# Performance work log

Measured on AMD Instinct MI355X. Metric: run time of the kernel, lower is better.

Reference implementation:

```python
import jax, jax.numpy as jnp
import numpy as np

V_FEATS = 1024; N1 = 800; N2 = 800; K = 10
CONV = [256, 128]; DENSE = [256, 64]


def setup_inputs() -> dict:
    key = jax.random.key(0)
    ks = jax.random.split(key, 20)
    inp = {
        "Z1": jax.random.normal(ks[0], (N1, V_FEATS), jnp.float32),
        "nb1": jax.random.randint(ks[2], (N1, K), -1, N1),
        "Z2": jax.random.normal(ks[1], (N2, V_FEATS), jnp.float32),
        "nb2": jax.random.randint(ks[3], (N2, K), -1, N2),
    }
    j = 4
    dims = [V_FEATS] + CONV
    for i, (di, do) in enumerate(zip(dims[:-1], dims[1:])):
        s = 1.0 / np.sqrt(di)
        inp[f"Wr{i}"] = jax.random.normal(ks[j], (di, do), jnp.float32) * s; j += 1
        inp[f"Wnr{i}"] = jax.random.normal(ks[j], (di, do), jnp.float32) * s; j += 1
    fdims = [2 * CONV[-1]] + DENSE + [1]
    for i, (di, do) in enumerate(zip(fdims[:-1], fdims[1:])):
        s = 1.0 / np.sqrt(di)
        inp[f"fW{i}"] = jax.random.normal(ks[j], (di, do), jnp.float32) * s; j += 1
        inp[f"fb{i}"] = jnp.zeros((do,), jnp.float32)
    return inp


def gnn_layer(Z, nb, Wr, Wnr):
    # residue (self) signal and neighbor base signal
    res = Z @ Wr                                  # [N, F]
    base = Z @ Wnr                                # [N, F]
    mask = nb > -1                                # [N, K]
    feats = base[nb] * mask[..., None]            # gather (neg idx wrap, masked out)
    norm = jnp.maximum(mask.sum(1), 1).astype(Z.dtype)  # [N], avoid div-by-0
    return jax.nn.relu(res + feats.sum(1) / norm[:, None])


def _forward(Z1, nb1, Z2, nb2, Wr0, Wnr0, Wr1, Wnr1, fW0, fb0, fW1, fb1, fW2, fb2):
    # two stacked GNN layers per protein (shared weights across the two proteins)
    x1 = gnn_layer(gnn_layer(Z1, nb1, Wr0, Wnr0), nb1, Wr1, Wnr1)  # [N1, F]
    x2 = gnn_layer(gnn_layer(Z2, nb2, Wr0, Wnr0), nb2, Wr1, Wnr1)  # [N2, F]
    n1, F = x1.shape
    n2 = x2.shape[0]
    # all-pairs concat: itertools.product(rows(x1), rows(x2)) -> [N1*N2, 2F]
    pairs = jnp.concatenate(
        [jnp.broadcast_to(x1[:, None, :], (n1, n2, F)),
         jnp.broadcast_to(x2[None, :, :], (n1, n2, F))], axis=-1
    ).reshape(n1 * n2, 2 * F)
    h = jax.nn.relu(pairs @ fW0 + fb0)
    h = jax.nn.relu(h @ fW1 + fb1)
    return jnp.squeeze(h @ fW2 + fb2)             # [N1*N2]


def reference(Z1, nb1, Z2, nb2, Wr0, Wnr0, Wr1, Wnr1, fW0, fb0, fW1, fb1, fW2, fb2):
    return _forward(Z1, nb1, Z2, nb2, Wr0, Wnr0, Wr1, Wnr1,
                    fW0, fb0, fW1, fb1, fW2, fb2)
```

## Files before the change

### kernel.cpp

```cpp
#include <hip/hip_runtime.h>
#include <hip/hip_bf16.h>
#include <cstdint>
#include <cstddef>


typedef __bf16 bf16_t;
typedef __bf16 bf16x8 __attribute__((ext_vector_type(8)));
typedef float f32x4 __attribute__((ext_vector_type(4)));
typedef _Float16 f16_t;
typedef _Float16 f16x8 __attribute__((ext_vector_type(8)));

static __device__ __forceinline__ f32x4 mfma_bf16(bf16x8 a, bf16x8 b, f32x4 c) {
  return __builtin_amdgcn_mfma_f32_16x16x32_bf16(a, b, c, 0, 0, 0);
}
static __device__ __forceinline__ f32x4 mfma_f16(f16x8 a, f16x8 b, f32x4 c) {
  return __builtin_amdgcn_mfma_f32_16x16x32_f16(a, b, c, 0, 0, 0);
}

#define N1R 800
#define NR  1600
#define VF  1024
#define F0  256
#define F1  128

__global__ void conv_w(const float* __restrict__ Wr0, const float* __restrict__ Wnr0,
                       const float* __restrict__ Wr1, const float* __restrict__ Wnr1,
                       const float* __restrict__ fW0, const float* __restrict__ fW1,
                       const float* __restrict__ fb1, const float* __restrict__ fW2,
                       const float* __restrict__ fb2,
                       bf16_t* __restrict__ W0h, bf16_t* __restrict__ W0l,
                       bf16_t* __restrict__ W1h, bf16_t* __restrict__ W1l,
                       bf16_t* __restrict__ fAh, bf16_t* __restrict__ fAl,
                       bf16_t* __restrict__ fBh, bf16_t* __restrict__ fBl,
                       f16_t* __restrict__ fW1th, float* __restrict__ fbw) {
  int wb = blockIdx.x;
  if (wb >= 2560 && wb < 2624) {
    int t = (wb - 2560) * 256 + threadIdx.x;
    int n = t & 63;
    int k = t >> 6;
    fW1th[(n << 8) + k] = (f16_t)fW1[k * 64 + n];
    return;
  }
  if (wb == 2624) {
    int t = threadIdx.x;
    if (t < 128) {
      int jl = t & 15, s = t >> 4;
      fbw[jl * 8 + s] = (s < 4) ? fb1[s * 16 + jl] : fW2[(s - 4) * 16 + jl];
    } else if (t == 128) {
      fbw[128] = fb2[0];
    }
    return;
  }
  const float* src; bf16_t* dh; bf16_t* dl; int ld, lk, ln, b0;
  if      (wb < 1024) { src = Wr0;  ld = 256; lk = 10; ln = 8; dh = W0h;              dl = W0l;              b0 = 0;    }
  else if (wb < 2048) { src = Wnr0; ld = 256; lk = 10; ln = 8; dh = W0h + 256 * 1024; dl = W0l + 256 * 1024; b0 = 1024; }
  else if (wb < 2176) { src = Wr1;  ld = 128; lk = 8;  ln = 7; dh = W1h;              dl = W1l;              b0 = 2048; }
  else if (wb < 2304) { src = Wnr1; ld = 128; lk = 8;  ln = 7; dh = W1h + 128 * 256;  dl = W1l + 128 * 256;  b0 = 2176; }
  else if (wb < 2432) { src = fW0;             ld = 256; lk = 7; ln = 8; dh = fAh;    dl = fAl;              b0 = 2304; }
  else                { src = fW0 + 128 * 256; ld = 256; lk = 7; ln = 8; dh = fBh;    dl = fBl;              b0 = 2432; }
  int t = (wb - b0) * 256 + threadIdx.x;
  int n = t & ((1 << ln) - 1);
  int k = t >> ln;
  float v = src[k * ld + n];
  bf16_t h = (bf16_t)v;
  dh[(n << lk) + k] = h;
  dl[(n << lk) + k] = (bf16_t)(v - (float)h);
}

static __device__ __forceinline__ void split8(float4 va, float4 vb,
                                              bf16x8& h8, bf16x8& l8) {
  float v[8] = {va.x, va.y, va.z, va.w, vb.x, vb.y, vb.z, vb.w};
  #pragma unroll
  for (int e = 0; e < 8; ++e) {
    bf16_t h = (bf16_t)v[e];
    h8[e] = h;
    l8[e] = (bf16_t)(v[e] - (float)h);
  }
}

__global__ __launch_bounds__(256) void gemm_z(
    const float* __restrict__ Z1, const float* __restrict__ Z2,
    const bf16_t* __restrict__ Bth, const bf16_t* __restrict__ Btl,
    float* __restrict__ Cp, int kLen) {
  int lane = threadIdx.x & 63;
  int w = threadIdx.x >> 6;
  int wr = w >> 1, wc = w & 1;
  int jl = lane & 15, hi = lane >> 4;

  int row0 = blockIdx.y * 64 + wr * 32;
  int col0 = blockIdx.x * 64 + wc * 32;
  int z = blockIdx.z;
  int kStart = z * kLen;
  float* C = Cp + (size_t)z * NR * 512;

  int r0 = row0 + jl;
  int r1 = row0 + 16 + jl;
  int c0 = col0 + jl;
  int c1 = col0 + 16 + jl;

  const float* pZ0 = ((r0 < N1R) ? Z1 + (size_t)r0 * VF : Z2 + (size_t)(r0 - N1R) * VF) + hi * 8;
  const float* pZ1 = ((r1 < N1R) ? Z1 + (size_t)r1 * VF : Z2 + (size_t)(r1 - N1R) * VF) + hi * 8;
  const bf16_t* pB0h = Bth + (size_t)c0 * 1024 + hi * 8;
  const bf16_t* pB1h = Bth + (size_t)c1 * 1024 + hi * 8;
  const bf16_t* pB0l = Btl + (size_t)c0 * 1024 + hi * 8;
  const bf16_t* pB1l = Btl + (size_t)c1 * 1024 + hi * 8;

  f32x4 acc[2][2] = {};
  for (int kb = kStart; kb < kStart + kLen; kb += 32) {
    bf16x8 a0h, a0l, a1h, a1l;
    split8(*(const float4*)(pZ0 + kb), *(const float4*)(pZ0 + kb + 4), a0h, a0l);
    split8(*(const float4*)(pZ1 + kb), *(const float4*)(pZ1 + kb + 4), a1h, a1l);
    bf16x8 b0h = *(const bf16x8*)(pB0h + kb);
    bf16x8 b1h = *(const bf16x8*)(pB1h + kb);
    bf16x8 b0l = *(const bf16x8*)(pB0l + kb);
    bf16x8 b1l = *(const bf16x8*)(pB1l + kb);

    acc[0][0] = mfma_bf16(a0h, b0h, acc[0][0]);
    acc[0][1] = mfma_bf16(a0h, b1h, acc[0][1]);
    acc[1][0] = mfma_bf16(a1h, b0h, acc[1][0]);
    acc[1][1] = mfma_bf16(a1h, b1h, acc[1][1]);

    acc[0][0] = mfma_bf16(a0l, b0h, acc[0][0]);
    acc[0][1] = mfma_bf16(a0l, b1h, acc[0][1]);
    acc[1][0] = mfma_bf16(a1l, b0h, acc[1][0]);
    acc[1][1] = mfma_bf16(a1l, b1h, acc[1][1]);

    acc[0][0] = mfma_bf16(a0h, b0l, acc[0][0]);
    acc[0][1] = mfma_bf16(a0h, b1l, acc[0][1]);
    acc[1][0] = mfma_bf16(a1h, b0l, acc[1][0]);
    acc[1][1] = mfma_bf16(a1h, b1l, acc[1][1]);
  }

  #pragma unroll
  for (int m = 0; m < 2; ++m) {
    #pragma unroll
    for (int nn = 0; nn < 2; ++nn) {
      int col = col0 + nn * 16 + jl;
      #pragma unroll
      for (int reg = 0; reg < 4; ++reg) {
        int row = row0 + m * 16 + hi * 4 + reg;
        C[(size_t)row * 512 + col] = acc[m][nn][reg];
      }
    }
  }
}

static __device__ __forceinline__ void gemm_body(
    const bf16_t* __restrict__ Ah, const bf16_t* __restrict__ Al,
    const bf16_t* __restrict__ Bth, const bf16_t* __restrict__ Btl,
    const float* __restrict__ bias, float* __restrict__ C,
    f16_t* __restrict__ Ch,
    int M, int N, int K, int kStart, int kLen, int row0b, int col0b) {
  int lane = threadIdx.x & 63;
  int w = threadIdx.x >> 6;
  int wr = w >> 1, wc = w & 1;
  int jl = lane & 15, hi = lane >> 4;

  int row0 = row0b + wr * 32;
  int col0 = col0b + wc * 32;

  int r0 = min(row0 + jl, M - 1);
  int r1 = min(row0 + 16 + jl, M - 1);
  int c0 = col0 + jl;
  int c1 = col0 + 16 + jl;

  const bf16_t* pA0h = Ah + (size_t)r0 * K + hi * 8;
  const bf16_t* pA1h = Ah + (size_t)r1 * K + hi * 8;
  const bf16_t* pA0l = Al + (size_t)r0 * K + hi * 8;
  const bf16_t* pA1l = Al + (size_t)r1 * K + hi * 8;
  const bf16_t* pB0h = Bth + (size_t)c0 * K + hi * 8;
  const bf16_t* pB1h = Bth + (size_t)c1 * K + hi * 8;
  const bf16_t* pB0l = Btl + (size_t)c0 * K + hi * 8;
  const bf16_t* pB1l = Btl + (size_t)c1 * K + hi * 8;

  f32x4 acc[2][2] = {};
  for (int kb = kStart; kb < kStart + kLen; kb += 32) {
    bf16x8 a0h = *(const bf16x8*)(pA0h + kb);
    bf16x8 a1h = *(const bf16x8*)(pA1h + kb);
    bf16x8 a0l = *(const bf16x8*)(pA0l + kb);
    bf16x8 a1l = *(const bf16x8*)(pA1l + kb);
    bf16x8 b0h = *(const bf16x8*)(pB0h + kb);
    bf16x8 b1h = *(const bf16x8*)(pB1h + kb);
    bf16x8 b0l = *(const bf16x8*)(pB0l + kb);
    bf16x8 b1l = *(const bf16x8*)(pB1l + kb);

    acc[0][0] = mfma_bf16(a0h, b0h, acc[0][0]);
    acc[0][1] = mfma_bf16(a0h, b1h, acc[0][1]);
    acc[1][0] = mfma_bf16(a1h, b0h, acc[1][0]);
    acc[1][1] = mfma_bf16(a1h, b1h, acc[1][1]);

    acc[0][0] = mfma_bf16(a0l, b0h, acc[0][0]);
    acc[0][1] = mfma_bf16(a0l, b1h, acc[0][1]);
    acc[1][0] = mfma_bf16(a1l, b0h, acc[1][0]);
    acc[1][1] = mfma_bf16(a1l, b1h, acc[1][1]);

    acc[0][0] = mfma_bf16(a0h, b0l, acc[0][0]);
    acc[0][1] = mfma_bf16(a0h, b1l, acc[0][1]);
    acc[1][0] = mfma_bf16(a1h, b0l, acc[1][0]);
    acc[1][1] = mfma_bf16(a1h, b1l, acc[1][1]);
  }

  #pragma unroll
  for (int m = 0; m < 2; ++m) {
    #pragma unroll
    for (int nn = 0; nn < 2; ++nn) {
      int col = col0 + nn * 16 + jl;
      float bv = bias ? bias[col] : 0.f;
      #pragma unroll
      for (int reg = 0; reg < 4; ++reg) {
        int row = row0 + m * 16 + hi * 4 + reg;
        if (row < M) {
          float val = acc[m][nn][reg] + bv;
          if (Ch) Ch[(size_t)row * N + col] = (f16_t)val;
          else    C[(size_t)row * N + col] = val;
        }
      }
    }
  }
}

__global__ __launch_bounds__(256) void gemm_split(
    const bf16_t* __restrict__ Ah, const bf16_t* __restrict__ Al,
    const bf16_t* __restrict__ Bth, const bf16_t* __restrict__ Btl,
    float* __restrict__ Cp, int M, int N, int K, int kLen) {
  int z = blockIdx.z;
  gemm_body(Ah, Al, Bth, Btl, nullptr, Cp + (size_t)z * M * N, nullptr,
            M, N, K, z * kLen, kLen, blockIdx.y * 64, blockIdx.x * 64);
}

__global__ __launch_bounds__(256) void gemm_dual(
    const bf16_t* __restrict__ H1h, const bf16_t* __restrict__ H1l,
    const bf16_t* __restrict__ fAh, const bf16_t* __restrict__ fAl,
    const bf16_t* __restrict__ fBh, const bf16_t* __restrict__ fBl,
    const float* __restrict__ fb0, f16_t* __restrict__ ABh) {
  int part = blockIdx.y / 13;
  int my = blockIdx.y % 13;
  gemm_body(H1h + (size_t)part * N1R * F1, H1l + (size_t)part * N1R * F1,
            part ? fBh : fAh, part ? fBl : fAl, part ? nullptr : fb0,
            nullptr, ABh + (size_t)part * N1R * 256, N1R, 256, F1, 0, F1,
            my * 64, blockIdx.x * 64);
}

__global__ void agg_kernel(const float* __restrict__ RBp, const int* __restrict__ nb1,
                           const int* __restrict__ nb2, bf16_t* __restrict__ Hh,
                           bf16_t* __restrict__ Hl, int F, int S) {
  int row = blockIdx.x;
  int c = threadIdx.x;
  int Sw = 2 * F;
  const size_t P = (size_t)NR * Sw;
  const int* nb;
  int roff;
  if (row < N1R) { nb = nb1 + row * 10; roff = 0; }
  else           { nb = nb2 + (row - N1R) * 10; roff = N1R; }
  float s = 0.f; int cnt = 0;
  #pragma unroll
  for (int k = 0; k < 10; ++k) {
    int idx = nb[k];
    if (idx > -1) {
      cnt++;
      size_t o = (size_t)(roff + idx) * Sw + F + c;
      float t = 0.f;
      for (int z = 0; z < S; ++z) t += RBp[o + (size_t)z * P];
      s += t;
    }
  }
  size_t so = (size_t)row * Sw + c;
  float v = 0.f;
  for (int z = 0; z < S; ++z) v += RBp[so + (size_t)z * P];
  v += s / (float)(cnt > 0 ? cnt : 1);
  v = fmaxf(v, 0.f);
  bf16_t h = (bf16_t)v;
  Hh[(size_t)row * F + c] = h;
  Hl[(size_t)row * F + c] = (bf16_t)(v - (float)h);
}

#define IBLK 2
#define ITILE 16
__global__ __launch_bounds__(256) void pair_kernel(
    const f16_t* __restrict__ ABh, const f16_t* __restrict__ W1th,
    const float* __restrict__ fbw, float* __restrict__ out) {
  __shared__ alignas(16) unsigned char sWh[64 * 512];
  __shared__ alignas(16) f16_t sA[ITILE * 256];

  const int tid = threadIdx.x;
  const int lane = tid & 63;
  const int w = tid >> 6;
  const int jl = lane & 15;
  const int hi = lane >> 4;
  const int j0 = blockIdx.x * 64;
  const int i0 = blockIdx.y * ITILE;

  #pragma unroll
  for (int s = 0; s < 8; ++s) {
    int c = tid + 256 * s;
    int n = c >> 5;
    int cb = (c & 31) << 4;
    int sw = cb ^ ((n & 7) << 4);
    *(uint4*)(sWh + n * 512 + sw) = *(const uint4*)((const unsigned char*)W1th + n * 512 + cb);
  }
  #pragma unroll
  for (int s = 0; s < 2; ++s) {
    int c = tid + 256 * s;
    int rr = c >> 5;
    int cc = c & 31;
    *(uint4*)((unsigned char*)sA + rr * 512 + cc * 16) =
        *(const uint4*)(ABh + (size_t)(i0 + rr) * 256 + cc * 8);
  }

  int j = j0 + w * 16 + jl;
  f16x8 breg[8];
  {
    const f16_t* Bp = ABh + (size_t)(N1R + j) * 256;
    bool ok = (j < N1R);
    f16x8 z{};
    #pragma unroll
    for (int t = 0; t < 8; ++t)
      breg[t] = ok ? *(const f16x8*)(Bp + t * 32 + hi * 8) : z;
  }

  float4 fb1r = *(const float4*)(fbw + jl * 8);
  float4 fw2r = *(const float4*)(fbw + jl * 8 + 4);
  float bias2 = fbw[128];

  __syncthreads();

  #pragma unroll 1
  for (int ig = 0; ig < ITILE / IBLK; ++ig) {
    f32x4 acc[IBLK][4] = {};
    #pragma unroll
    for (int t = 0; t < 8; ++t) {
      f16x8 bv = breg[t];
      f16x8 af[IBLK];
      const f16x8 Zv{};
      #pragma unroll
      for (int ib = 0; ib < IBLK; ++ib) {
        f16x8 av = *(const f16x8*)(sA + (ig * IBLK + ib) * 256 + t * 32 + hi * 8);
        af[ib] = __builtin_elementwise_max(av + bv, Zv);
      }
      int kbyte = t * 64 + hi * 16;
      #pragma unroll
      for (int nf = 0; nf < 4; ++nf) {
        int n = nf * 16 + jl;
        f16x8 wh = *(const f16x8*)(sWh + n * 512 + (kbyte ^ ((n & 7) << 4)));
        #pragma unroll
        for (int ib = 0; ib < IBLK; ++ib)
          acc[ib][nf] = mfma_f16(af[ib], wh, acc[ib][nf]);
      }
    }
    float fb1a[4] = {fb1r.x, fb1r.y, fb1r.z, fb1r.w};
    float fw2a[4] = {fw2r.x, fw2r.y, fw2r.z, fw2r.w};
    #pragma unroll
    for (int ib = 0; ib < IBLK; ++ib) {
      float part[4];
      #pragma unroll
      for (int r = 0; r < 4; ++r) {
        float ssum = 0.f;
        #pragma unroll
        for (int nf = 0; nf < 4; ++nf) {
          float h = acc[ib][nf][r] + fb1a[nf];
          h = fmaxf(h, 0.f);
          ssum += h * fw2a[nf];
        }
        part[r] = ssum;
      }
      #pragma unroll
      for (int off = 1; off < 16; off <<= 1) {
        #pragma unroll
        for (int r = 0; r < 4; ++r) part[r] += __shfl_xor(part[r], off, 64);
      }
      if (jl == 0) {
        int jo = j0 + w * 16 + hi * 4;
        if (jo < N1R) {
          float4 o = make_float4(part[0] + bias2, part[1] + bias2,
                                 part[2] + bias2, part[3] + bias2);
          *(float4*)(out + (size_t)(i0 + ig * IBLK + ib) * 800 + jo) = o;
        }
      }
    }
  }
}

extern "C" void kernel_launch(void* const* d_in, const int* in_sizes, int n_in,
                              void* d_out, int out_size, void* d_ws, size_t ws_size,
                              hipStream_t stream) {
  const float* Z1   = (const float*)d_in[0];
  const int*   nb1  = (const int*)d_in[1];
  const float* Z2   = (const float*)d_in[2];
  const int*   nb2  = (const int*)d_in[3];
  const float* Wr0  = (const float*)d_in[4];
  const float* Wnr0 = (const float*)d_in[5];
  const float* Wr1  = (const float*)d_in[6];
  const float* Wnr1 = (const float*)d_in[7];
  const float* fW0  = (const float*)d_in[8];
  const float* fb0  = (const float*)d_in[9];
  const float* fW1  = (const float*)d_in[10];
  const float* fb1  = (const float*)d_in[11];
  const float* fW2  = (const float*)d_in[12];
  const float* fb2  = (const float*)d_in[13];
  float* out = (float*)d_out;

  char* p = (char*)d_ws;
  auto alloc = [&](size_t bytes) {
    char* q = p;
    p += (bytes + 255) & ~(size_t)255;
    return q;
  };
  bf16_t* W0h   = (bf16_t*)alloc((size_t)512 * 1024 * 2);
  bf16_t* W0l   = (bf16_t*)alloc((size_t)512 * 1024 * 2);
  bf16_t* W1h   = (bf16_t*)alloc((size_t)256 * 256 * 2);
  bf16_t* W1l   = (bf16_t*)alloc((size_t)256 * 256 * 2);
  bf16_t* fAh   = (bf16_t*)alloc((size_t)256 * 128 * 2);
  bf16_t* fAl   = (bf16_t*)alloc((size_t)256 * 128 * 2);
  bf16_t* fBh   = (bf16_t*)alloc((size_t)256 * 128 * 2);
  bf16_t* fBl   = (bf16_t*)alloc((size_t)256 * 128 * 2);
  f16_t*  fW1th = (f16_t*)alloc((size_t)64 * 256 * 2);
  float*  fbw   = (float*)alloc(129 * 4);
  bf16_t* H0h   = (bf16_t*)alloc((size_t)NR * F0 * 2);
  bf16_t* H0l   = (bf16_t*)alloc((size_t)NR * F0 * 2);
  bf16_t* H1h   = (bf16_t*)alloc((size_t)NR * F1 * 2);
  bf16_t* H1l   = (bf16_t*)alloc((size_t)NR * F1 * 2);
  f16_t*  ABh   = (f16_t*)alloc((size_t)NR * 256 * 2);
  size_t part1 = (size_t)NR * 512 * 4;
  size_t part2 = (size_t)NR * 256 * 4;
  size_t used = (size_t)(p - (char*)d_ws);
  int S = 1, S2 = 1;
  if (used + 4 * part1 + 4 * part2 + 2048 <= ws_size) { S = 4; S2 = 4; }
  else if (used + 2 * part1 + 2 * part2 + 2048 <= ws_size) { S = 2; S2 = 2; }
  float* RB0p = (float*)alloc(S * part1);
  float* RB1p = (float*)alloc(S2 * part2);
  (void)in_sizes; (void)n_in; (void)out_size;

  conv_w<<<2625, 256, 0, stream>>>(Wr0, Wnr0, Wr1, Wnr1, fW0, fW1, fb1, fW2, fb2,
                                   W0h, W0l, W1h, W1l, fAh, fAl, fBh, fBl,
                                   fW1th, fbw);
  gemm_z<<<dim3(8, 25, S), 256, 0, stream>>>(Z1, Z2, W0h, W0l, RB0p, 1024 / S);
  agg_kernel<<<NR, 256, 0, stream>>>(RB0p, nb1, nb2, H0h, H0l, F0, S);
  gemm_split<<<dim3(4, 25, S2), 256, 0, stream>>>(H0h, H0l, W1h, W1l, RB1p,
                                                  NR, 256, 256, 256 / S2);
  agg_kernel<<<NR, 128, 0, stream>>>(RB1p, nb1, nb2, H1h, H1l, F1, S2);
  gemm_dual<<<dim3(4, 26), 256, 0, stream>>>(H1h, H1l, fAh, fAl, fBh, fBl, fb0, ABh);
  pair_kernel<<<dim3(13, 50), 256, 0, stream>>>(ABh, fW1th, fbw, out);
}
```

Baseline: 119.5 us.

## Aggregate neighbours before the GEMM and fuse residual/neighbour GEMMs with ReLU epilogue

Uses linearity to reorder each GNN layer: neighbour inputs are averaged first (Z or H0 gathered and mean-pooled), then a single K-concatenated GEMM multiplies [self, aggregated] by [Wr; Wnr]. ReLU and the hi/lo bf16 split move into the GEMM epilogue. This removes the split-K partial buffers, the fp32 [N,512] and [N,256] intermediates, and the separate agg pass over those partials. In exchange it adds a gather over the 1024-wide input Z inside the weight-conversion kernel and writes a bf16 hi/lo copy of the aggregated Z. It also drops the split-K parallelism, so the layer-1 GEMM runs with fewer blocks and a longer K loop.

```diff
diff --git a/kernel.cpp b/kernel.cpp
--- a/kernel.cpp
+++ b/kernel.cpp
@@ -5,6 +5,7 @@
 
 
 typedef __bf16 bf16_t;
+typedef __bf16 bf16x4 __attribute__((ext_vector_type(4)));
 typedef __bf16 bf16x8 __attribute__((ext_vector_type(8)));
 typedef float f32x4 __attribute__((ext_vector_type(4)));
 typedef _Float16 f16_t;
@@ -23,30 +24,75 @@
 #define F0  256
 #define F1  128
 
-__global__ void conv_w(const float* __restrict__ Wr0, const float* __restrict__ Wnr0,
-                       const float* __restrict__ Wr1, const float* __restrict__ Wnr1,
-                       const float* __restrict__ fW0, const float* __restrict__ fW1,
-                       const float* __restrict__ fb1, const float* __restrict__ fW2,
-                       const float* __restrict__ fb2,
-                       bf16_t* __restrict__ W0h, bf16_t* __restrict__ W0l,
-                       bf16_t* __restrict__ W1h, bf16_t* __restrict__ W1l,
-                       bf16_t* __restrict__ fAh, bf16_t* __restrict__ fAl,
-                       bf16_t* __restrict__ fBh, bf16_t* __restrict__ fBl,
-                       f16_t* __restrict__ fW1th, float* __restrict__ fbw) {
+static __device__ __forceinline__ void split8(float4 va, float4 vb,
+                                              bf16x8& h8, bf16x8& l8) {
+  float v[8] = {va.x, va.y, va.z, va.w, vb.x, vb.y, vb.z, vb.w};
+  #pragma unroll
+  for (int e = 0; e < 8; ++e) {
+    bf16_t h = (bf16_t)v[e];
+    h8[e] = h;
+    l8[e] = (bf16_t)(v[e] - (float)h);
+  }
+}
+
+__global__ void conv_agg(const float* __restrict__ Z1, const float* __restrict__ Z2,
+                         const int* __restrict__ nb1, const int* __restrict__ nb2,
+                         const float* __restrict__ Wr0, const float* __restrict__ Wnr0,
+                         const float* __restrict__ Wr1, const float* __restrict__ Wnr1,
+                         const float* __restrict__ fW0, const float* __restrict__ fW1,
+                         const float* __restrict__ fb1, const float* __restrict__ fW2,
+                         const float* __restrict__ fb2,
+                         bf16_t* __restrict__ W0h, bf16_t* __restrict__ W0l,
+                         bf16_t* __restrict__ W1h, bf16_t* __restrict__ W1l,
+                         bf16_t* __restrict__ fAh, bf16_t* __restrict__ fAl,
+                         bf16_t* __restrict__ fBh, bf16_t* __restrict__ fBl,
+                         f16_t* __restrict__ fW1th, float* __restrict__ fbw,
+                         bf16_t* __restrict__ Zah, bf16_t* __restrict__ Zal) {
   int wb = blockIdx.x;
+  int tid = threadIdx.x;
+  if (wb >= 2625) {
+    int r = wb - 2625;
+    const int* nbp;
+    const float* Zp;
+    if (r < N1R) { nbp = nb1 + r * 10; Zp = Z1; }
+    else         { nbp = nb2 + (r - N1R) * 10; Zp = Z2; }
+    int c4 = tid * 4;
+    float4 s = make_float4(0.f, 0.f, 0.f, 0.f);
+    int cnt = 0;
+    #pragma unroll
+    for (int k = 0; k < 10; ++k) {
+      int idx = nbp[k];
+      if (idx > -1) {
+        cnt++;
+        float4 v = *(const float4*)(Zp + (size_t)idx * VF + c4);
+        s.x += v.x; s.y += v.y; s.z += v.z; s.w += v.w;
+      }
+    }
+    float inv = 1.f / (float)(cnt > 0 ? cnt : 1);
+    float vv[4] = {s.x * inv, s.y * inv, s.z * inv, s.w * inv};
+    bf16x4 h4, l4;
+    #pragma unroll
+    for (int e = 0; e < 4; ++e) {
+      bf16_t h = (bf16_t)vv[e];
+      h4[e] = h;
+      l4[e] = (bf16_t)(vv[e] - (float)h);
+    }
+    *(bf16x4*)(Zah + (size_t)r * VF + c4) = h4;
+    *(bf16x4*)(Zal + (size_t)r * VF + c4) = l4;
+    return;
+  }
   if (wb >= 2560 && wb < 2624) {
-    int t = (wb - 2560) * 256 + threadIdx.x;
+    int t = (wb - 2560) * 256 + tid;
     int n = t & 63;
     int k = t >> 6;
     fW1th[(n << 8) + k] = (f16_t)fW1[k * 64 + n];
     return;
   }
   if (wb == 2624) {
-    int t = threadIdx.x;
-    if (t < 128) {
-      int jl = t & 15, s = t >> 4;
+    if (tid < 128) {
+      int jl = tid & 15, s = tid >> 4;
       fbw[jl * 8 + s] = (s < 4) ? fb1[s * 16 + jl] : fW2[(s - 4) * 16 + jl];
-    } else if (t == 128) {
+    } else if (tid == 128) {
       fbw[128] = fb2[0];
     }
     return;
@@ -58,7 +104,7 @@
   else if (wb < 2304) { src = Wnr1; ld = 128; lk = 8;  ln = 7; dh = W1h + 128 * 256;  dl = W1l + 128 * 256;  b0 = 2176; }
   else if (wb < 2432) { src = fW0;             ld = 256; lk = 7; ln = 8; dh = fAh;    dl = fAl;              b0 = 2304; }
   else                { src = fW0 + 128 * 256; ld = 256; lk = 7; ln = 8; dh = fBh;    dl = fBl;              b0 = 2432; }
-  int t = (wb - b0) * 256 + threadIdx.x;
+  int t = (wb - b0) * 256 + tid;
   int n = t & ((1 << ln) - 1);
   int k = t >> ln;
   float v = src[k * ld + n];
@@ -67,80 +113,155 @@
   dl[(n << lk) + k] = (bf16_t)(v - (float)h);
 }
 
-static __device__ __forceinline__ void split8(float4 va, float4 vb,
-                                              bf16x8& h8, bf16x8& l8) {
-  float v[8] = {va.x, va.y, va.z, va.w, vb.x, vb.y, vb.z, vb.w};
-  #pragma unroll
-  for (int e = 0; e < 8; ++e) {
-    bf16_t h = (bf16_t)v[e];
-    h8[e] = h;
-    l8[e] = (bf16_t)(v[e] - (float)h);
-  }
-}
-
-__global__ __launch_bounds__(256) void gemm_z(
+#define STEP6(ah, al, b0h, b0l, b1h, b1l)        \
+  acc0 = mfma_bf16(ah, b0h, acc0);               \
+  acc1 = mfma_bf16(ah, b1h, acc1);               \
+  acc0 = mfma_bf16(al, b0h, acc0);               \
+  acc1 = mfma_bf16(al, b1h, acc1);               \
+  acc0 = mfma_bf16(ah, b0l, acc0);               \
+  acc1 = mfma_bf16(ah, b1l, acc1);
+
+__global__ __launch_bounds__(256) void gemm_l1(
     const float* __restrict__ Z1, const float* __restrict__ Z2,
-    const bf16_t* __restrict__ Bth, const bf16_t* __restrict__ Btl,
-    float* __restrict__ Cp, int kLen) {
+    const bf16_t* __restrict__ Zah, const bf16_t* __restrict__ Zal,
+    const bf16_t* __restrict__ W0h, const bf16_t* __restrict__ W0l,
+    bf16_t* __restrict__ H0h, bf16_t* __restrict__ H0l) {
   int lane = threadIdx.x & 63;
   int w = threadIdx.x >> 6;
   int wr = w >> 1, wc = w & 1;
   int jl = lane & 15, hi = lane >> 4;
 
-  int row0 = blockIdx.y * 64 + wr * 32;
+  int row0 = blockIdx.y * 32 + wr * 16;
   int col0 = blockIdx.x * 64 + wc * 32;
-  int z = blockIdx.z;
-  int kStart = z * kLen;
-  float* C = Cp + (size_t)z * NR * 512;
-
-  int r0 = row0 + jl;
-  int r1 = row0 + 16 + jl;
-  int c0 = col0 + jl;
-  int c1 = col0 + 16 + jl;
-
-  const float* pZ0 = ((r0 < N1R) ? Z1 + (size_t)r0 * VF : Z2 + (size_t)(r0 - N1R) * VF) + hi * 8;
-  const float* pZ1 = ((r1 < N1R) ? Z1 + (size_t)r1 * VF : Z2 + (size_t)(r1 - N1R) * VF) + hi * 8;
-  const bf16_t* pB0h = Bth + (size_t)c0 * 1024 + hi * 8;
-  const bf16_t* pB1h = Bth + (size_t)c1 * 1024 + hi * 8;
-  const bf16_t* pB0l = Btl + (size_t)c0 * 1024 + hi * 8;
-  const bf16_t* pB1l = Btl + (size_t)c1 * 1024 + hi * 8;
-
-  f32x4 acc[2][2] = {};
-  for (int kb = kStart; kb < kStart + kLen; kb += 32) {
-    bf16x8 a0h, a0l, a1h, a1l;
-    split8(*(const float4*)(pZ0 + kb), *(const float4*)(pZ0 + kb + 4), a0h, a0l);
-    split8(*(const float4*)(pZ1 + kb), *(const float4*)(pZ1 + kb + 4), a1h, a1l);
+  int r = row0 + jl;
+  int c0 = col0 + jl, c1 = col0 + 16 + jl;
+
+  const float* pZ = ((r < N1R) ? Z1 + (size_t)r * VF
+                               : Z2 + (size_t)(r - N1R) * VF) + hi * 8;
+  const bf16_t* pAh = Zah + (size_t)r * VF + hi * 8;
+  const bf16_t* pAl = Zal + (size_t)r * VF + hi * 8;
+  const bf16_t* pB0h = W0h + (size_t)c0 * 1024 + hi * 8;
+  const bf16_t* pB1h = W0h + (size_t)c1 * 1024 + hi * 8;
+  const bf16_t* pB0l = W0l + (size_t)c0 * 1024 + hi * 8;
+  const bf16_t* pB1l = W0l + (size_t)c1 * 1024 + hi * 8;
+  const size_t OFF = (size_t)256 * 1024;
+
+  f32x4 acc0 = {}, acc1 = {};
+  for (int kb = 0; kb < 1024; kb += 32) {
+    bf16x8 ah, al;
+    split8(*(const float4*)(pZ + kb), *(const float4*)(pZ + kb + 4), ah, al);
     bf16x8 b0h = *(const bf16x8*)(pB0h + kb);
     bf16x8 b1h = *(const bf16x8*)(pB1h + kb);
     bf16x8 b0l = *(const bf16x8*)(pB0l + kb);
     bf16x8 b1l = *(const bf16x8*)(pB1l + kb);
-
-    acc[0][0] = mfma_bf16(a0h, b0h, acc[0][0]);
-    acc[0][1] = mfma_bf16(a0h, b1h, acc[0][1]);
-    acc[1][0] = mfma_bf16(a1h, b0h, acc[1][0]);
-    acc[1][1] = mfma_bf16(a1h, b1h, acc[1][1]);
-
-    acc[0][0] = mfma_bf16(a0l, b0h, acc[0][0]);
-    acc[0][1] = mfma_bf16(a0l, b1h, acc[0][1]);
-    acc[1][0] = mfma_bf16(a1l, b0h, acc[1][0]);
-    acc[1][1] = mfma_bf16(a1l, b1h, acc[1][1]);
-
-    acc[0][0] = mfma_bf16(a0h, b0l, acc[0][0]);
-    acc[0][1] = mfma_bf16(a0h, b1l, acc[0][1]);
-    acc[1][0] = mfma_bf16(a1h, b0l, acc[1][0]);
-    acc[1][1] = mfma_bf16(a1h, b1l, acc[1][1]);
-  }
-
-  #pragma unroll
-  for (int m = 0; m < 2; ++m) {
-    #pragma unroll
-    for (int nn = 0; nn < 2; ++nn) {
-      int col = col0 + nn * 16 + jl;
-      #pragma unroll
-      for (int reg = 0; reg < 4; ++reg) {
-        int row = row0 + m * 16 + hi * 4 + reg;
-        C[(size_t)row * 512 + col] = acc[m][nn][reg];
-      }
+    STEP6(ah, al, b0h, b0l, b1h, b1l)
+  }
+  for (int kb = 0; kb < 1024; kb += 32) {
+    bf16x8 ah = *(const bf16x8*)(pAh + kb);
+    bf16x8 al = *(const bf16x8*)(pAl + kb);
+    bf16x8 b0h = *(const bf16x8*)(pB0h + OFF + kb);
+    bf16x8 b1h = *(const bf16x8*)(pB1h + OFF + kb);
+    bf16x8 b0l = *(const bf16x8*)(pB0l + OFF + kb);
+    bf16x8 b1l = *(const bf16x8*)(pB1l + OFF + kb);
+    STEP6(ah, al, b0h, b0l, b1h, b1l)
+  }
+
+  f32x4 accs[2] = {acc0, acc1};
+  #pragma unroll
+  for (int nn = 0; nn < 2; ++nn) {
+    int col = col0 + nn * 16 + jl;
+    #pragma unroll
+    for (int reg = 0; reg < 4; ++reg) {
+      int row = row0 + hi * 4 + reg;
+      float v = fmaxf(accs[nn][reg], 0.f);
+      bf16_t h = (bf16_t)v;
+      H0h[(size_t)row * F0 + col] = h;
+      H0l[(size_t)row * F0 + col] = (bf16_t)(v - (float)h);
+    }
+  }
+}
+
+__global__ void agg1_kernel(const bf16_t* __restrict__ H0h, const bf16_t* __restrict__ H0l,
+                            const int* __restrict__ nb1, const int* __restrict__ nb2,
+                            bf16_t* __restrict__ Gah, bf16_t* __restrict__ Gal) {
+  int r = blockIdx.x;
+  int c = threadIdx.x;
+  const int* nbp;
+  int roff;
+  if (r < N1R) { nbp = nb1 + r * 10; roff = 0; }
+  else         { nbp = nb2 + (r - N1R) * 10; roff = N1R; }
+  float s = 0.f; int cnt = 0;
+  #pragma unroll
+  for (int k = 0; k < 10; ++k) {
+    int idx = nbp[k];
+    if (idx > -1) {
+      cnt++;
+      size_t o = (size_t)(roff + idx) * F0 + c;
+      s += (float)H0h[o] + (float)H0l[o];
+    }
+  }
+  float v = s / (float)(cnt > 0 ? cnt : 1);
+  bf16_t h = (bf16_t)v;
+  Gah[(size_t)r * F0 + c] = h;
+  Gal[(size_t)r * F0 + c] = (bf16_t)(v - (float)h);
+}
+
+__global__ __launch_bounds__(256) void gemm_l2(
+    const bf16_t* __restrict__ H0h, const bf16_t* __restrict__ H0l,
+    const bf16_t* __restrict__ Gah, const bf16_t* __restrict__ Gal,
+    const bf16_t* __restrict__ W1h, const bf16_t* __restrict__ W1l,
+    bf16_t* __restrict__ H1h, bf16_t* __restrict__ H1l) {
+  int lane = threadIdx.x & 63;
+  int w = threadIdx.x >> 6;
+  int wr = w >> 1, wc = w & 1;
+  int jl = lane & 15, hi = lane >> 4;
+
+  int row0 = blockIdx.y * 32 + wr * 16;
+  int col0 = blockIdx.x * 64 + wc * 32;
+  int r = row0 + jl;
+  int c0 = col0 + jl, c1 = col0 + 16 + jl;
+
+  const bf16_t* pAh = H0h + (size_t)r * F0 + hi * 8;
+  const bf16_t* pAl = H0l + (size_t)r * F0 + hi * 8;
+  const bf16_t* pGh = Gah + (size_t)r * F0 + hi * 8;
+  const bf16_t* pGl = Gal + (size_t)r * F0 + hi * 8;
+  const bf16_t* pB0h = W1h + (size_t)c0 * 256 + hi * 8;
+  const bf16_t* pB1h = W1h + (size_t)c1 * 256 + hi * 8;
+  const bf16_t* pB0l = W1l + (size_t)c0 * 256 + hi * 8;
+  const bf16_t* pB1l = W1l + (size_t)c1 * 256 + hi * 8;
+  const size_t OFF = (size_t)128 * 256;
+
+  f32x4 acc0 = {}, acc1 = {};
+  for (int kb = 0; kb < 256; kb += 32) {
+    bf16x8 ah = *(const bf16x8*)(pAh + kb);
+    bf16x8 al = *(const bf16x8*)(pAl + kb);
+    bf16x8 b0h = *(const bf16x8*)(pB0h + kb);
+    bf16x8 b1h = *(const bf16x8*)(pB1h + kb);
+    bf16x8 b0l = *(const bf16x8*)(pB0l + kb);
+    bf16x8 b1l = *(const bf16x8*)(pB1l + kb);
+    STEP6(ah, al, b0h, b0l, b1h, b1l)
+  }
+  for (int kb = 0; kb < 256; kb += 32) {
+    bf16x8 ah = *(const bf16x8*)(pGh + kb);
+    bf16x8 al = *(const bf16x8*)(pGl + kb);
+    bf16x8 b0h = *(const bf16x8*)(pB0h + OFF + kb);
+    bf16x8 b1h = *(const bf16x8*)(pB1h + OFF + kb);
+    bf16x8 b0l = *(const bf16x8*)(pB0l + OFF + kb);
+    bf16x8 b1l = *(const bf16x8*)(pB1l + OFF + kb);
+    STEP6(ah, al, b0h, b0l, b1h, b1l)
+  }
+
+  f32x4 accs[2] = {acc0, acc1};
+  #pragma unroll
+  for (int nn = 0; nn < 2; ++nn) {
+    int col = col0 + nn * 16 + jl;
+    #pragma unroll
+    for (int reg = 0; reg < 4; ++reg) {
+      int row = row0 + hi * 4 + reg;
+      float v = fmaxf(accs[nn][reg], 0.f);
+      bf16_t h = (bf16_t)v;
+      H1h[(size_t)row * F1 + col] = h;
+      H1l[(size_t)row * F1 + col] = (bf16_t)(v - (float)h);
     }
   }
 }
@@ -148,9 +269,8 @@
 static __device__ __forceinline__ void gemm_body(
     const bf16_t* __restrict__ Ah, const bf16_t* __restrict__ Al,
     const bf16_t* __restrict__ Bth, const bf16_t* __restrict__ Btl,
-    const float* __restrict__ bias, float* __restrict__ C,
-    f16_t* __restrict__ Ch,
-    int M, int N, int K, int kStart, int kLen, int row0b, int col0b) {
+    const float* __restrict__ bias, f16_t* __restrict__ Ch,
+    int M, int N, int K, int row0b, int col0b) {
   int lane = threadIdx.x & 63;
   int w = threadIdx.x >> 6;
   int wr = w >> 1, wc = w & 1;
@@ -174,7 +294,7 @@
   const bf16_t* pB1l = Btl + (size_t)c1 * K + hi * 8;
 
   f32x4 acc[2][2] = {};
-  for (int kb = kStart; kb < kStart + kLen; kb += 32) {
+  for (int kb = 0; kb < K; kb += 32) {
     bf16x8 a0h = *(const bf16x8*)(pA0h + kb);
     bf16x8 a1h = *(const bf16x8*)(pA1h + kb);
     bf16x8 a0l = *(const bf16x8*)(pA0l + kb);
@@ -209,23 +329,10 @@
       #pragma unroll
       for (int reg = 0; reg < 4; ++reg) {
         int row = row0 + m * 16 + hi * 4 + reg;
-        if (row < M) {
-          float val = acc[m][nn][reg] + bv;
-          if (Ch) Ch[(size_t)row * N + col] = (f16_t)val;
-          else    C[(size_t)row * N + col] = val;
-        }
-      }
-    }
-  }
-}
-
-__global__ __launch_bounds__(256) void gemm_split(
-    const bf16_t* __restrict__ Ah, const bf16_t* __restrict__ Al,
-    const bf16_t* __restrict__ Bth, const bf16_t* __restrict__ Btl,
-    float* __restrict__ Cp, int M, int N, int K, int kLen) {
-  int z = blockIdx.z;
-  gemm_body(Ah, Al, Bth, Btl, nullptr, Cp + (size_t)z * M * N, nullptr,
-            M, N, K, z * kLen, kLen, blockIdx.y * 64, blockIdx.x * 64);
+        if (row < M) Ch[(size_t)row * N + col] = (f16_t)(acc[m][nn][reg] + bv);
+      }
+    }
+  }
 }
 
 __global__ __launch_bounds__(256) void gemm_dual(
@@ -237,41 +344,8 @@
   int my = blockIdx.y % 13;
   gemm_body(H1h + (size_t)part * N1R * F1, H1l + (size_t)part * N1R * F1,
             part ? fBh : fAh, part ? fBl : fAl, part ? nullptr : fb0,
-            nullptr, ABh + (size_t)part * N1R * 256, N1R, 256, F1, 0, F1,
+            ABh + (size_t)part * N1R * 256, N1R, 256, F1,
             my * 64, blockIdx.x * 64);
-}
-
-__global__ void agg_kernel(const float* __restrict__ RBp, const int* __restrict__ nb1,
-                           const int* __restrict__ nb2, bf16_t* __restrict__ Hh,
-                           bf16_t* __restrict__ Hl, int F, int S) {
-  int row = blockIdx.x;
-  int c = threadIdx.x;
-  int Sw = 2 * F;
-  const size_t P = (size_t)NR * Sw;
-  const int* nb;
-  int roff;
-  if (row < N1R) { nb = nb1 + row * 10; roff = 0; }
-  else           { nb = nb2 + (row - N1R) * 10; roff = N1R; }
-  float s = 0.f; int cnt = 0;
-  #pragma unroll
-  for (int k = 0; k < 10; ++k) {
-    int idx = nb[k];
-    if (idx > -1) {
-      cnt++;
-      size_t o = (size_t)(roff + idx) * Sw + F + c;
-      float t = 0.f;
-      for (int z = 0; z < S; ++z) t += RBp[o + (size_t)z * P];
-      s += t;
-    }
-  }
-  size_t so = (size_t)row * Sw + c;
-  float v = 0.f;
-  for (int z = 0; z < S; ++z) v += RBp[so + (size_t)z * P];
-  v += s / (float)(cnt > 0 ? cnt : 1);
-  v = fmaxf(v, 0.f);
-  bf16_t h = (bf16_t)v;
-  Hh[(size_t)row * F + c] = h;
-  Hl[(size_t)row * F + c] = (bf16_t)(v - (float)h);
 }
 
 #define IBLK 2
@@ -415,29 +489,24 @@
   bf16_t* fBl   = (bf16_t*)alloc((size_t)256 * 128 * 2);
   f16_t*  fW1th = (f16_t*)alloc((size_t)64 * 256 * 2);
   float*  fbw   = (float*)alloc(129 * 4);
+  bf16_t* Zah   = (bf16_t*)alloc((size_t)NR * VF * 2);
+  bf16_t* Zal   = (bf16_t*)alloc((size_t)NR * VF * 2);
   bf16_t* H0h   = (bf16_t*)alloc((size_t)NR * F0 * 2);
   bf16_t* H0l   = (bf16_t*)alloc((size_t)NR * F0 * 2);
+  bf16_t* Gah   = (bf16_t*)alloc((size_t)NR * F0 * 2);
+  bf16_t* Gal   = (bf16_t*)alloc((size_t)NR * F0 * 2);
   bf16_t* H1h   = (bf16_t*)alloc((size_t)NR * F1 * 2);
   bf16_t* H1l   = (bf16_t*)alloc((size_t)NR * F1 * 2);
   f16_t*  ABh   = (f16_t*)alloc((size_t)NR * 256 * 2);
-  size_t part1 = (size_t)NR * 512 * 4;
-  size_t part2 = (size_t)NR * 256 * 4;
-  size_t used = (size_t)(p - (char*)d_ws);
-  int S = 1, S2 = 1;
-  if (used + 4 * part1 + 4 * part2 + 2048 <= ws_size) { S = 4; S2 = 4; }
-  else if (used + 2 * part1 + 2 * part2 + 2048 <= ws_size) { S = 2; S2 = 2; }
-  float* RB0p = (float*)alloc(S * part1);
-  float* RB1p = (float*)alloc(S2 * part2);
-  (void)in_sizes; (void)n_in; (void)out_size;
-
-  conv_w<<<2625, 256, 0, stream>>>(Wr0, Wnr0, Wr1, Wnr1, fW0, fW1, fb1, fW2, fb2,
-                                   W0h, W0l, W1h, W1l, fAh, fAl, fBh, fBl,
-                                   fW1th, fbw);
-  gemm_z<<<dim3(8, 25, S), 256, 0, stream>>>(Z1, Z2, W0h, W0l, RB0p, 1024 / S);
-  agg_kernel<<<NR, 256, 0, stream>>>(RB0p, nb1, nb2, H0h, H0l, F0, S);
-  gemm_split<<<dim3(4, 25, S2), 256, 0, stream>>>(H0h, H0l, W1h, W1l, RB1p,
-                                                  NR, 256, 256, 256 / S2);
-  agg_kernel<<<NR, 128, 0, stream>>>(RB1p, nb1, nb2, H1h, H1l, F1, S2);
+  (void)in_sizes; (void)n_in; (void)out_size; (void)ws_size;
+
+  conv_agg<<<4225, 256, 0, stream>>>(Z1, Z2, nb1, nb2, Wr0, Wnr0, Wr1, Wnr1,
+                                     fW0, fW1, fb1, fW2, fb2,
+                                     W0h, W0l, W1h, W1l, fAh, fAl, fBh, fBl,
+                                     fW1th, fbw, Zah, Zal);
+  gemm_l1<<<dim3(4, 50), 256, 0, stream>>>(Z1, Z2, Zah, Zal, W0h, W0l, H0h, H0l);
+  agg1_kernel<<<NR, 256, 0, stream>>>(H0h, H0l, nb1, nb2, Gah, Gal);
+  gemm_l2<<<dim3(2, 50), 256, 0, stream>>>(H0h, H0l, Gah, Gal, W1h, W1l, H1h, H1l);
   gemm_dual<<<dim3(4, 26), 256, 0, stream>>>(H1h, H1l, fAh, fAl, fBh, fBl, fb0, ABh);
   pair_kernel<<<dim3(13, 50), 256, 0, stream>>>(ABh, fW1th, fbw, out);
 }
```

Measured after the change: 120.4 us. About the same (+0.7%).
